# Kernel tuning notes

Hardware: AMD Instinct MI355X
Metric: run time of the kernel (lower is better)

The kernel has to match this reference:

```python
import jax, jax.numpy as jnp
import numpy as np

TEMPERATURE = 0.05
EPS = 1e-8  # F.cosine_similarity default eps


def setup_inputs() -> dict:
    key = jax.random.key(0)
    k1, k2 = jax.random.split(key)
    N, D = 8192, 256
    return {
        "query_embeddings": jax.random.normal(k1, (N, D), dtype=jnp.float32),
        "pos_embeddings": jax.random.normal(k2, (N, D), dtype=jnp.float32),
    }


def _normalize(x):
    # matches F.cosine_similarity: x / max(||x||, eps)
    norm = jnp.sqrt(jnp.sum(x * x, axis=-1, keepdims=True))
    return x / jnp.maximum(norm, EPS)


def reference(query_embeddings, pos_embeddings):
    q = _normalize(query_embeddings)  # [N, D]
    p = _normalize(pos_embeddings)    # [N, D]
    # cosine similarity matrix via GEMM instead of (N,N,D) broadcast
    sim = jnp.einsum("nd,md->nm", q, p) / TEMPERATURE  # [N, N]
    # cross-entropy with labels = arange(N): loss_i = logsumexp(sim_i) - sim_ii
    logz = jax.nn.logsumexp(sim, axis=-1)  # [N]
    diag = jnp.diagonal(sim)               # [N]
    loss = jnp.mean(logz - diag)
    return loss
```

## Files before the change

kernel.cpp:

```cpp
#include <hip/hip_runtime.h>
#include <hip/hip_bf16.h>

#define NROWS 8192
#define DDIM  256
#define INV_TEMP 20.0f

typedef __attribute__((ext_vector_type(8))) short bf16x8;
typedef __attribute__((ext_vector_type(4))) float f32x4;

__device__ static inline void async16(const void* g, void* l) {
    __builtin_amdgcn_global_load_lds(
        (const __attribute__((address_space(1))) void*)g,
        (__attribute__((address_space(3))) void*)l, 16, 0, 0);
}

__global__ __launch_bounds__(256) void norm_diag_kernel(
    const float* __restrict__ q, const float* __restrict__ p,
    unsigned short* __restrict__ qn, unsigned short* __restrict__ pn,
    float* __restrict__ diag, float* __restrict__ lse,
    unsigned int* __restrict__ counter)
{
    const int row  = blockIdx.x * 4 + (threadIdx.x >> 6);
    const int lane = threadIdx.x & 63;

    const float4 qv = ((const float4*)(q + (size_t)row * DDIM))[lane];
    const float4 pv = ((const float4*)(p + (size_t)row * DDIM))[lane];

    float sq = qv.x*qv.x + qv.y*qv.y + qv.z*qv.z + qv.w*qv.w;
    float sp = pv.x*pv.x + pv.y*pv.y + pv.z*pv.z + pv.w*pv.w;
    #pragma unroll
    for (int m = 1; m < 64; m <<= 1) {
        sq += __shfl_xor(sq, m);
        sp += __shfl_xor(sp, m);
    }
    const float qs = 1.0f / fmaxf(sqrtf(sq), 1e-8f);
    const float ps = 1.0f / fmaxf(sqrtf(sp), 1e-8f);

    const float qx = qv.x*qs, qy = qv.y*qs, qz = qv.z*qs, qw = qv.w*qs;
    const float px = pv.x*ps, py = pv.y*ps, pz = pv.z*ps, pw = pv.w*ps;

    float d = qx*px + qy*py + qz*pz + qw*pw;
    #pragma unroll
    for (int m = 1; m < 64; m <<= 1) d += __shfl_xor(d, m);
    if (lane == 0) {
        diag[row] = d * INV_TEMP;
        lse[row]  = 0.0f;
    }
    if (blockIdx.x == 0 && threadIdx.x == 0) *counter = 0u;

    union { unsigned short u16[4]; uint2 v; } uq, up;
    {
        __hip_bfloat16 b;
        b = __float2bfloat16(qx); uq.u16[0] = *(unsigned short*)&b;
        b = __float2bfloat16(qy); uq.u16[1] = *(unsigned short*)&b;
        b = __float2bfloat16(qz); uq.u16[2] = *(unsigned short*)&b;
        b = __float2bfloat16(qw); uq.u16[3] = *(unsigned short*)&b;
        b = __float2bfloat16(px); up.u16[0] = *(unsigned short*)&b;
        b = __float2bfloat16(py); up.u16[1] = *(unsigned short*)&b;
        b = __float2bfloat16(pz); up.u16[2] = *(unsigned short*)&b;
        b = __float2bfloat16(pw); up.u16[3] = *(unsigned short*)&b;
    }
    *(uint2*)(qn + (size_t)row * DDIM + lane * 4) = uq.v;
    *(uint2*)(pn + (size_t)row * DDIM + lane * 4) = up.v;
}

__global__ __launch_bounds__(256, 2) void simexp_kernel(
    const unsigned short* __restrict__ qn,
    const unsigned short* __restrict__ pn,
    float* __restrict__ lse, const float* __restrict__ diag,
    unsigned int* __restrict__ counter, float* __restrict__ out)
{
    __shared__ unsigned char lds[32768];
    __shared__ float wsum[4];
    __shared__ unsigned int is_last;

    const int tid  = threadIdx.x;
    const int lane = tid & 63;
    const int w    = tid >> 6;
    const int quad = lane >> 4;
    const int l16  = lane & 15;
    const int rowbase  = blockIdx.y * 128;
    const int colstart = blockIdx.x * 1024;
    const int rowstart = rowbase + w * 32;

    bf16x8 a[2][8];
    #pragma unroll
    for (int rt = 0; rt < 2; ++rt)
        #pragma unroll
        for (int ks = 0; ks < 8; ++ks)
            a[rt][ks] = *(const bf16x8*)(qn +
                (size_t)(rowstart + rt * 16 + l16) * DDIM + ks * 32 + quad * 8);

    const unsigned short* sB = pn +
        (size_t)(colstart + w * 16 + l16) * DDIM + quad * 8;

    float lsum[2][4];
    #pragma unroll
    for (int rt = 0; rt < 2; ++rt)
        #pragma unroll
        for (int r = 0; r < 4; ++r) lsum[rt][r] = 0.0f;

    for (int c = 0; c < 16; ++c) {
        __syncthreads();
        #pragma unroll
        for (int st = 0; st < 8; ++st)
            async16(sB + c * 16384 + st * 32, lds + w * 8192 + st * 1024);
        __syncthreads();

        f32x4 acc[2][4];
        #pragma unroll
        for (int rt = 0; rt < 2; ++rt)
            #pragma unroll
            for (int ct = 0; ct < 4; ++ct) acc[rt][ct] = (f32x4)0.0f;

        #pragma unroll
        for (int ks = 0; ks < 8; ++ks) {
            bf16x8 bf[4];
            #pragma unroll
            for (int ct = 0; ct < 4; ++ct)
                bf[ct] = *(const bf16x8*)(lds +
                    ct * 8192 + ks * 1024 + quad * 256 + l16 * 16);
            #pragma unroll
            for (int ct = 0; ct < 4; ++ct)
                #pragma unroll
                for (int rt = 0; rt < 2; ++rt)
                    acc[rt][ct] = __builtin_amdgcn_mfma_f32_16x16x32_bf16(
                        a[rt][ks], bf[ct], acc[rt][ct], 0, 0, 0);
        }

        #pragma unroll
        for (int rt = 0; rt < 2; ++rt)
            #pragma unroll
            for (int r = 0; r < 4; ++r)
                lsum[rt][r] += __expf(acc[rt][0][r] * INV_TEMP)
                             + __expf(acc[rt][1][r] * INV_TEMP)
                             + __expf(acc[rt][2][r] * INV_TEMP)
                             + __expf(acc[rt][3][r] * INV_TEMP);
    }

    #pragma unroll
    for (int rt = 0; rt < 2; ++rt)
        #pragma unroll
        for (int r = 0; r < 4; ++r) {
            float s = lsum[rt][r];
            s += __shfl_xor(s, 1);
            s += __shfl_xor(s, 2);
            s += __shfl_xor(s, 4);
            s += __shfl_xor(s, 8);
            if (l16 == 0)
                atomicAdd(&lse[rowstart + rt * 16 + quad * 4 + r], s);
        }

    __threadfence();
    __syncthreads();
    if (tid == 0) {
        const unsigned int nblk = gridDim.x * gridDim.y;
        is_last = (atomicAdd(counter, 1u) == nblk - 1u);
    }
    __syncthreads();
    if (is_last) {
        __threadfence();
        float s = 0.0f;
        for (int i = tid; i < NROWS; i += 256) {
            float v = __hip_atomic_load(&lse[i], __ATOMIC_RELAXED,
                                        __HIP_MEMORY_SCOPE_AGENT);
            s += __logf(v) - diag[i];
        }
        #pragma unroll
        for (int m = 1; m < 64; m <<= 1) s += __shfl_xor(s, m);
        if (lane == 0) wsum[w] = s;
        __syncthreads();
        if (tid == 0)
            out[0] = (wsum[0] + wsum[1] + wsum[2] + wsum[3]) * (1.0f / NROWS);
    }
}

extern "C" void kernel_launch(void* const* d_in, const int* in_sizes, int n_in,
                              void* d_out, int out_size, void* d_ws, size_t ws_size,
                              hipStream_t stream)
{
    const float* q = (const float*)d_in[0];
    const float* p = (const float*)d_in[1];

    char* ws = (char*)d_ws;
    unsigned short* qn = (unsigned short*)ws;
    unsigned short* pn = (unsigned short*)(ws + (size_t)NROWS*DDIM*2);
    float* diag = (float*)(ws + 2 * (size_t)NROWS * DDIM * 2);
    float* lse  = diag + NROWS;
    unsigned int* counter = (unsigned int*)(lse + NROWS);

    norm_diag_kernel<<<NROWS / 4, 256, 0, stream>>>(q, p, qn, pn, diag, lse, counter);

    dim3 grid(8, 64);
    simexp_kernel<<<grid, 256, 0, stream>>>(qn, pn, lse, diag, counter, (float*)d_out);
}
```

Baseline: 147.3 us.

## Pre-swizzle bf16 operands into MFMA fragment layout and use 32x32 MFMA without LDS

The normalize kernel now writes q and p in a fragment-blocked layout, so each lane can load one contiguous 16-byte MFMA operand straight from global memory. The similarity kernel drops the LDS staging and its barriers and streams B fragments from global/L2 through a 4-deep register prefetch ring. It switches from 16x16x32 to 32x32x16 MFMA with 64 rows per wave, and the grid changes to 16x32. This removes LDS traffic and synchronisation but relies on L2 to serve the B fragments each wave reads, and raises register pressure with 32 A fragments and four 16-wide accumulators per wave.

After: 151.0 us. +2.5%, slower.

```diff
diff --git a/kernel.cpp b/kernel.cpp
--- a/kernel.cpp
+++ b/kernel.cpp
@@ -5,14 +5,9 @@
 #define DDIM  256
 #define INV_TEMP 20.0f
 
-typedef __attribute__((ext_vector_type(8))) short bf16x8;
-typedef __attribute__((ext_vector_type(4))) float f32x4;
+typedef __attribute__((ext_vector_type(8)))  short bf16x8;
+typedef __attribute__((ext_vector_type(16))) float f32x16;
 
-__device__ static inline void async16(const void* g, void* l) {
-    __builtin_amdgcn_global_load_lds(
-        (const __attribute__((address_space(1))) void*)g,
-        (__attribute__((address_space(3))) void*)l, 16, 0, 0);
-}
 
 __global__ __launch_bounds__(256) void norm_diag_kernel(
     const float* __restrict__ q, const float* __restrict__ p,
@@ -60,8 +55,12 @@
         b = __float2bfloat16(pz); up.u16[2] = *(unsigned short*)&b;
         b = __float2bfloat16(pw); up.u16[3] = *(unsigned short*)&b;
     }
-    *(uint2*)(qn + (size_t)row * DDIM + lane * 4) = uq.v;
-    *(uint2*)(pn + (size_t)row * DDIM + lane * 4) = up.v;
+    const int s = lane >> 2, h = (lane >> 1) & 1;
+    const int cb = row >> 5, c = row & 31;
+    const size_t dst = ((size_t)(s * 256 + cb) << 10) + (h << 9) + (c << 4)
+                     + ((lane & 1) << 3);
+    *(uint2*)((char*)qn + dst) = uq.v;
+    *(uint2*)((char*)pn + dst) = up.v;
 }
 
 __global__ __launch_bounds__(256, 2) void simexp_kernel(
@@ -70,86 +69,63 @@
     float* __restrict__ lse, const float* __restrict__ diag,
     unsigned int* __restrict__ counter, float* __restrict__ out)
 {
-    __shared__ unsigned char lds[32768];
     __shared__ float wsum[4];
     __shared__ unsigned int is_last;
 
     const int tid  = threadIdx.x;
     const int lane = tid & 63;
     const int w    = tid >> 6;
-    const int quad = lane >> 4;
-    const int l16  = lane & 15;
-    const int rowbase  = blockIdx.y * 128;
-    const int colstart = blockIdx.x * 1024;
-    const int rowstart = rowbase + w * 32;
+    const int rowstart = blockIdx.y * 256 + w * 64;
+    const int cbA = rowstart >> 5;
+    const int cb0 = blockIdx.x * 16;
 
-    bf16x8 a[2][8];
+    bf16x8 a0[16], a1[16];
     #pragma unroll
-    for (int rt = 0; rt < 2; ++rt)
-        #pragma unroll
-        for (int ks = 0; ks < 8; ++ks)
-            a[rt][ks] = *(const bf16x8*)(qn +
-                (size_t)(rowstart + rt * 16 + l16) * DDIM + ks * 32 + quad * 8);
+    for (int s = 0; s < 16; ++s) {
+        a0[s] = *(const bf16x8*)(qn + (size_t)(s * 256 + cbA    ) * 512 + lane * 8);
+        a1[s] = *(const bf16x8*)(qn + (size_t)(s * 256 + cbA + 1) * 512 + lane * 8);
+    }
 
-    const unsigned short* sB = pn +
-        (size_t)(colstart + w * 16 + l16) * DDIM + quad * 8;
+    const unsigned short* bbase = pn + lane * 8;
+    #define FRAG(f) (*(const bf16x8*)(bbase + \
+        (size_t)((((f) & 15) * 256) + cb0 + ((f) >> 4)) * 512))
 
-    float lsum[2][4];
-    #pragma unroll
-    for (int rt = 0; rt < 2; ++rt)
-        #pragma unroll
-        for (int r = 0; r < 4; ++r) lsum[rt][r] = 0.0f;
+    bf16x8 bq[4] = { FRAG(0), FRAG(1), FRAG(2), FRAG(3) };
+
+    f32x16 lsum0 = (f32x16)0.0f, lsum1 = (f32x16)0.0f;
 
     for (int c = 0; c < 16; ++c) {
-        __syncthreads();
+        f32x16 acc0 = (f32x16)0.0f, acc1 = (f32x16)0.0f;
         #pragma unroll
-        for (int st = 0; st < 8; ++st)
-            async16(sB + c * 16384 + st * 32, lds + w * 8192 + st * 1024);
-        __syncthreads();
-
-        f32x4 acc[2][4];
+        for (int s = 0; s < 16; ++s) {
+            bf16x8 cur = bq[s & 3];
+            const int f = c * 16 + s + 4;
+            if (f < 256) bq[s & 3] = FRAG(f);
+            acc0 = __builtin_amdgcn_mfma_f32_32x32x16_bf16(a0[s], cur, acc0, 0, 0, 0);
+            acc1 = __builtin_amdgcn_mfma_f32_32x32x16_bf16(a1[s], cur, acc1, 0, 0, 0);
+        }
         #pragma unroll
-        for (int rt = 0; rt < 2; ++rt)
-            #pragma unroll
-            for (int ct = 0; ct < 4; ++ct) acc[rt][ct] = (f32x4)0.0f;
-
-        #pragma unroll
-        for (int ks = 0; ks < 8; ++ks) {
-            bf16x8 bf[4];
-            #pragma unroll
-            for (int ct = 0; ct < 4; ++ct)
-                bf[ct] = *(const bf16x8*)(lds +
-                    ct * 8192 + ks * 1024 + quad * 256 + l16 * 16);
-            #pragma unroll
-            for (int ct = 0; ct < 4; ++ct)
-                #pragma unroll
-                for (int rt = 0; rt < 2; ++rt)
-                    acc[rt][ct] = __builtin_amdgcn_mfma_f32_16x16x32_bf16(
-                        a[rt][ks], bf[ct], acc[rt][ct], 0, 0, 0);
+        for (int r = 0; r < 16; ++r) {
+            lsum0[r] += __expf(acc0[r] * INV_TEMP);
+            lsum1[r] += __expf(acc1[r] * INV_TEMP);
         }
-
-        #pragma unroll
-        for (int rt = 0; rt < 2; ++rt)
-            #pragma unroll
-            for (int r = 0; r < 4; ++r)
-                lsum[rt][r] += __expf(acc[rt][0][r] * INV_TEMP)
-                             + __expf(acc[rt][1][r] * INV_TEMP)
-                             + __expf(acc[rt][2][r] * INV_TEMP)
-                             + __expf(acc[rt][3][r] * INV_TEMP);
     }
+    #undef FRAG
 
     #pragma unroll
-    for (int rt = 0; rt < 2; ++rt)
+    for (int r = 0; r < 16; ++r) {
+        float v0 = lsum0[r], v1 = lsum1[r];
         #pragma unroll
-        for (int r = 0; r < 4; ++r) {
-            float s = lsum[rt][r];
-            s += __shfl_xor(s, 1);
-            s += __shfl_xor(s, 2);
-            s += __shfl_xor(s, 4);
-            s += __shfl_xor(s, 8);
-            if (l16 == 0)
-                atomicAdd(&lse[rowstart + rt * 16 + quad * 4 + r], s);
+        for (int m = 1; m < 32; m <<= 1) {
+            v0 += __shfl_xor(v0, m);
+            v1 += __shfl_xor(v1, m);
         }
+        if ((lane & 31) == 0) {
+            const int rl = (r & 3) + 8 * (r >> 2) + ((lane >> 5) << 2);
+            atomicAdd(&lse[rowstart + rl],      v0);
+            atomicAdd(&lse[rowstart + 32 + rl], v1);
+        }
+    }
 
     __threadfence();
     __syncthreads();
@@ -191,6 +167,6 @@
 
     norm_diag_kernel<<<NROWS / 4, 256, 0, stream>>>(q, p, qn, pn, diag, lse, counter);
 
-    dim3 grid(8, 64);
+    dim3 grid(16, 32);
     simexp_kernel<<<grid, 256, 0, stream>>>(qn, pn, lse, diag, counter, (float*)d_out);
 }
```
